# Kernel optimization log

Measured on AMD Instinct MI355X. Metric: run time of the kernel, lower is better.

The kernel has to match this reference:

```python
import jax, jax.numpy as jnp
import numpy as np

B, C, H, W = 2, 320, 48, 48
HEADS, DIM_HEAD, NUM_FILTERS = 8, 64, 32
INNER = HEADS * DIM_HEAD  # 512
LN_EPS = 1e-05


def setup_inputs() -> dict:
    key = jax.random.key(0)
    ks = jax.random.split(key, 8)
    w = 0.02
    return {
        "hidden_states": jax.random.normal(ks[0], (B, C, H, W), jnp.float32),
        "encoder_hidden_states": jax.random.normal(ks[1], (B, C, H, W), jnp.float32),
        "Wq": jax.random.normal(ks[2], (C, INNER), jnp.float32) * w,
        "Wk": jax.random.normal(ks[3], (C, INNER), jnp.float32) * w,
        "Wv": jax.random.normal(ks[4], (C, INNER), jnp.float32) * w,
        "Wo": jax.random.normal(ks[5], (INNER, C), jnp.float32) * w,
        "bo": jnp.zeros((C,), jnp.float32),
        "ln_gamma": jnp.ones((C,), jnp.float32),
        "ln_beta": jnp.zeros((C,), jnp.float32),
        "ex_filters": jax.random.normal(ks[6], (NUM_FILTERS, INNER), jnp.float32),
        "dist_filters": jax.random.normal(ks[7], (NUM_FILTERS, INNER), jnp.float32),
        "scale": jnp.ones((1,), jnp.float32),  # learnable scale shadows dim_head**-0.5
    }


def _split_heads(t, heads):
    b, s, d = t.shape
    return t.reshape(b, s, heads, d // heads).transpose(0, 2, 1, 3)  # [b,h,s,dh]


def reference(hidden_states, encoder_hidden_states, Wq, Wk, Wv, Wo, bo,
              ln_gamma, ln_beta, ex_filters, dist_filters, scale):
    b, c, h, w = hidden_states.shape
    _, _, rh, rw = encoder_hidden_states.shape
    residual = hidden_states
    s = scale[0]

    hs = hidden_states.transpose(0, 2, 3, 1).reshape(b, h * w, c)        # [b, q, C]
    ehs = encoder_hidden_states.transpose(0, 2, 3, 1).reshape(b, rh * rw, c)

    # LayerNorm on encoder states
    mu = ehs.mean(-1, keepdims=True)
    var = jnp.mean((ehs - mu) ** 2, axis=-1, keepdims=True)
    ehs = (ehs - mu) * jax.lax.rsqrt(var + LN_EPS) * ln_gamma + ln_beta

    q = _split_heads(hs @ Wq, HEADS)    # [b,h,q,dh]
    k = _split_heads(ehs @ Wk, HEADS)   # [b,h,kv,dh]
    v = _split_heads(ehs @ Wv, HEADS)   # [b,h,kv,dh]
    ef = _split_heads(jnp.broadcast_to(ex_filters[None], (b,) + ex_filters.shape), HEADS)   # [b,h,F,dh]
    df = _split_heads(jnp.broadcast_to(dist_filters[None], (b,) + dist_filters.shape), HEADS)

    # spatial attention: softmax over kv positions
    spatial = jax.nn.softmax(jnp.einsum('bhfd,bhkd->bhfk', ef, k) * s, axis=-1)   # [b,h,F,kv]
    # channel attention: softmax over the filter axis (torch dim=1 of [B*h, F, q])
    channel = jax.nn.softmax(jnp.einsum('bhfd,bhqd->bhfq', df, q) * s, axis=2)    # [b,h,F,q]

    attn = jnp.einsum('bhfq,bhfk->bhqk', channel, spatial)                        # [b,h,q,kv]
    out = jnp.einsum('bhqk,bhkd->bhqd', attn, v)                                  # [b,h,q,dh]

    out = out.transpose(0, 2, 1, 3).reshape(b, h * w, INNER)
    out = out @ Wo + bo
    out = out.reshape(b, h, w, c).transpose(0, 3, 1, 2)
    return out + residual * s
```

## Files before the change

### kernel.cpp

```cpp
#include <hip/hip_runtime.h>
#include <math.h>

#define Bc 2
#define Cc 320
#define Pc 2304
#define HEADSc 8
#define DHc 64
#define INNERc 512
#define Fc 32
#define LN_EPS 1e-5f
#define CHUNKS 36
#define CHUNK_P 64

typedef __attribute__((ext_vector_type(8))) short bf16x8;
typedef __attribute__((ext_vector_type(4))) float f32x4;

static __device__ __forceinline__ ushort f2bf(float x) {
  uint u = __builtin_bit_cast(uint, x);
  u = (u + 0x7fffu + ((u >> 16) & 1u)) >> 16;
  return (ushort)u;
}

static __device__ __forceinline__ void gload16(const ushort* g, ushort* l) {
  __builtin_amdgcn_global_load_lds(
      (const __attribute__((address_space(1))) uint*)g,
      (__attribute__((address_space(3))) uint*)l, 16, 0, 0);
}

static __device__ void transpose_tile(const float* __restrict__ src,
                                      ushort* __restrict__ dst, int R, int C,
                                      int r0, int c0, int tid,
                                      float (*t)[65]) {
#pragma unroll
  for (int it = 0; it < 4; ++it) {
    int lin = it * 256 + tid;
    int rr = lin >> 4, c4 = lin & 15;
    float4 v = *(const float4*)(&src[(size_t)(r0 + rr) * C + c0 + c4 * 4]);
    t[rr][c4 * 4 + 0] = v.x; t[rr][c4 * 4 + 1] = v.y;
    t[rr][c4 * 4 + 2] = v.z; t[rr][c4 * 4 + 3] = v.w;
  }
  __syncthreads();
#pragma unroll
  for (int it = 0; it < 2; ++it) {
    int lin = it * 256 + tid;
    int cc = lin >> 3, r8 = lin & 7;
    ushort tmp[8];
#pragma unroll
    for (int j = 0; j < 8; ++j) tmp[j] = f2bf(t[r8 * 8 + j][cc]);
    *(uint4*)(&dst[(size_t)(c0 + cc) * R + r0 + r8 * 8]) = *(const uint4*)tmp;
  }
}

__global__ __launch_bounds__(256) void prep_all_kernel(
    const float* __restrict__ hs, const float* __restrict__ ehs,
    const float* __restrict__ gamma, const float* __restrict__ beta,
    const float* __restrict__ Wv, const float* __restrict__ Wo,
    const float* __restrict__ exf, const float* __restrict__ Wk,
    const float* __restrict__ dif, const float* __restrict__ Wq,
    ushort* __restrict__ hsT, ushort* __restrict__ ehsT,
    ushort* __restrict__ WvT, ushort* __restrict__ WoT,
    ushort* __restrict__ Gk, ushort* __restrict__ Gq) {
  __shared__ float smem[6448];
  int idx = blockIdx.x, tid = threadIdx.x;

  if (idx < 144) {
    int pt = idx % 36, z = idx / 36;
    int b = z & 1, which = z >> 1;
    int pos0 = pt * 64;
    const float* src = (which ? ehs : hs) + (size_t)b * Cc * Pc;
    ushort* dst = (which ? ehsT : hsT) + (size_t)b * Pc * Cc;
    float* t = smem;
    float* s1 = smem + 4160;
    float* s2 = smem + 4416;
    float* lmean = smem + 4672;
    float* lrstd = smem + 4736;
    int lane = tid & 63, g = tid >> 6;
    if (which) {
      const float* base = src + pos0 + lane;
      float sum = 0.f, sq = 0.f;
      for (int c = g * 80; c < g * 80 + 80; ++c) {
        float x = base[(size_t)c * Pc];
        sum += x; sq += x * x;
      }
      s1[g * 64 + lane] = sum; s2[g * 64 + lane] = sq;
      __syncthreads();
      if (tid < 64) {
        float ts = s1[tid] + s1[64 + tid] + s1[128 + tid] + s1[192 + tid];
        float tq = s2[tid] + s2[64 + tid] + s2[128 + tid] + s2[192 + tid];
        float mean = ts / (float)Cc;
        float var = tq / (float)Cc - mean * mean;
        lmean[tid] = mean;
        lrstd[tid] = rsqrtf(var + LN_EPS);
      }
      __syncthreads();
    }
    float4 pv[4];
#pragma unroll
    for (int it = 0; it < 4; ++it) {
      int lin = it * 256 + tid, rr = lin >> 4, c4 = lin & 15;
      pv[it] = *(const float4*)(&src[(size_t)rr * Pc + pos0 + c4 * 4]);
    }
    for (int ct = 0; ct < 5; ++ct) {
      int r0 = ct * 64;
#pragma unroll
      for (int it = 0; it < 4; ++it) {
        int lin = it * 256 + tid, rr = lin >> 4, c4 = lin & 15;
        t[rr * 65 + c4 * 4 + 0] = pv[it].x;
        t[rr * 65 + c4 * 4 + 1] = pv[it].y;
        t[rr * 65 + c4 * 4 + 2] = pv[it].z;
        t[rr * 65 + c4 * 4 + 3] = pv[it].w;
      }
      __syncthreads();
      if (ct < 4) {
#pragma unroll
        for (int it = 0; it < 4; ++it) {
          int lin = it * 256 + tid, rr = lin >> 4, c4 = lin & 15;
          pv[it] =
              *(const float4*)(&src[(size_t)(r0 + 64 + rr) * Pc + pos0 + c4 * 4]);
        }
      }
#pragma unroll
      for (int it = 0; it < 2; ++it) {
        int lin = it * 256 + tid;
        int cc = lin >> 3, r8 = lin & 7;
        float m_ = which ? lmean[cc] : 0.f, rs_ = which ? lrstd[cc] : 1.f;
        ushort tmp[8];
#pragma unroll
        for (int j = 0; j < 8; ++j) {
          int ch = r8 * 8 + j;
          float x = t[ch * 65 + cc];
          float val = which ? (x - m_) * rs_ * gamma[r0 + ch] + beta[r0 + ch] : x;
          tmp[j] = f2bf(val);
        }
        *(uint4*)(&dst[(size_t)(pos0 + cc) * Cc + r0 + r8 * 8]) =
            *(const uint4*)tmp;
      }
      __syncthreads();
    }
  } else {
    int idx2 = idx - 144;
    if (idx2 < 40) {
      transpose_tile(Wv, WvT, Cc, INNERc, (idx2 / 8) * 64, (idx2 % 8) * 64,
                     tid, (float(*)[65])smem);
    } else if (idx2 < 80) {
      int i = idx2 - 40;
      transpose_tile(Wo, WoT, INNERc, Cc, (i / 5) * 64, (i % 5) * 64, tid,
                     (float(*)[65])smem);
    } else {
      int i = idx2 - 80;
      int c0 = (i % 5) * 64, h = (i / 5) % 8, zz = i / 40;
      const float* filt = zz ? dif : exf;
      const float* W = zz ? Wq : Wk;
      ushort* G = zz ? Gq : Gk;
      float (*ef)[66] = (float(*)[66])smem;
      float (*wk)[65] = (float(*)[65])(smem + 32 * 66);
      for (int l = tid; l < Fc * DHc; l += 256) {
        int f = l >> 6, d = l & 63;
        ef[f][d] = filt[(size_t)f * INNERc + h * 64 + d];
      }
      for (int l = tid; l < 64 * DHc; l += 256) {
        int cc = l >> 6, d = l & 63;
        wk[cc][d] = W[(size_t)(c0 + cc) * INNERc + h * 64 + d];
      }
      __syncthreads();
      int f = tid >> 3, cbase = tid & 7;
      float acc[8] = {};
#pragma unroll
      for (int d4 = 0; d4 < DHc; d4 += 4) {
        float4 a = *(const float4*)(&ef[f][d4]);
#pragma unroll
        for (int j = 0; j < 8; ++j) {
          float4 b = *(const float4*)(&wk[cbase + j * 8][d4]);
          acc[j] += a.x * b.x + a.y * b.y + a.z * b.z + a.w * b.w;
        }
      }
#pragma unroll
      for (int j = 0; j < 8; ++j)
        G[(size_t)(h * Fc + f) * Cc + c0 + cbase + j * 8] = f2bf(acc[j]);
    }
  }
}

__global__ __launch_bounds__(256) void spatial_kernel(
    const ushort* __restrict__ Gk, const ushort* __restrict__ ehsT,
    const ushort* __restrict__ WvT, const float* __restrict__ scale_p,
    float* __restrict__ svp, float* __restrict__ mj, float* __restrict__ lj) {
  int c = blockIdx.x, h = blockIdx.y, b = blockIdx.z;
  int tid = threadIdx.x, lane = tid & 63, wv = tid >> 6;
  int l15 = lane & 15, kq = lane >> 4;
  int pos0 = c * CHUNK_P;
  int bh = b * HEADSc + h;
  float s = scale_p[0];

  __shared__ alignas(16) char smem[40960];
  float* Sq = (float*)smem;
  ushort* Vs = (ushort*)(smem + 8704);
  ushort* P = (ushort*)(smem + 17920);

  const ushort* Av = WvT + (size_t)(h * 64) * Cc;
  const ushort* Ag = Gk + (size_t)(h * Fc) * Cc;
  const ushort* Bb = ehsT + ((size_t)b * Pc + pos0) * Cc;

  auto stage = [&](int buf, int k0) {
    ushort* As_ = (ushort*)(smem + buf * 20480);
    ushort* Bs_ = (ushort*)(smem + buf * 20480 + 12288);
#pragma unroll
    for (int it = 0; it < 3; ++it) {
      int lin = it * 256 + tid;
      int row = lin >> 3, p = lin & 7;
      int lc = p ^ (row & 7);
      const ushort* sp = (row < 64)
                             ? (Av + (size_t)row * Cc + k0 + lc * 8)
                             : (Ag + (size_t)(row - 64) * Cc + k0 + lc * 8);
      gload16(sp, &As_[lin * 8]);
    }
#pragma unroll
    for (int it = 0; it < 2; ++it) {
      int lin = it * 256 + tid;
      int row = lin >> 3, p = lin & 7;
      int lc = p ^ (row & 7);
      gload16(Bb + (size_t)row * Cc + k0 + lc * 8, &Bs_[lin * 8]);
    }
  };

  f32x4 acc[6] = {};
  stage(0, 0);
  __syncthreads();
  int cur = 0;
  for (int t = 0; t < 5; ++t) {
    if (t < 4) stage(cur ^ 1, (t + 1) * 64);
    const ushort* As_ = (const ushort*)(smem + cur * 20480);
    const ushort* Bs_ = (const ushort*)(smem + cur * 20480 + 12288);
#pragma unroll
    for (int ss = 0; ss < 2; ++ss) {
      bf16x8 af[6], bfr;
#pragma unroll
      for (int mt = 0; mt < 6; ++mt) {
        int m = mt * 16 + l15;
        int p = (ss * 4 + kq) ^ (m & 7);
        af[mt] = *(const bf16x8*)(&As_[m * 64 + p * 8]);
      }
      {
        int n = wv * 16 + l15;
        int p = (ss * 4 + kq) ^ (n & 7);
        bfr = *(const bf16x8*)(&Bs_[n * 64 + p * 8]);
      }
#pragma unroll
      for (int mt = 0; mt < 6; ++mt)
        acc[mt] = __builtin_amdgcn_mfma_f32_16x16x32_bf16(af[mt], bfr, acc[mt],
                                                          0, 0, 0);
    }
    __syncthreads();
    cur ^= 1;
  }
#pragma unroll
  for (int mt = 0; mt < 6; ++mt) {
    int col = wv * 16 + l15;
#pragma unroll
    for (int r = 0; r < 4; ++r) {
      int row = mt * 16 + kq * 4 + r;
      if (mt < 4) Vs[row * 72 + col] = f2bf(acc[mt][r]);
      else Sq[(row - 64) * 68 + col] = acc[mt][r];
    }
  }
  __syncthreads();

  {
    int row = tid >> 3, sub = tid & 7;
    float vals[8];
    float m_ = -1e30f;
#pragma unroll
    for (int i = 0; i < 8; ++i) {
      vals[i] = s * Sq[row * 68 + sub * 8 + i];
      m_ = fmaxf(m_, vals[i]);
    }
    m_ = fmaxf(m_, __shfl_xor(m_, 1));
    m_ = fmaxf(m_, __shfl_xor(m_, 2));
    m_ = fmaxf(m_, __shfl_xor(m_, 4));
    float l_ = 0.f;
#pragma unroll
    for (int i = 0; i < 8; i += 2) {
      float e0 = __expf(vals[i] - m_);
      float e1 = __expf(vals[i + 1] - m_);
      l_ += e0 + e1;
      uint pk = (uint)f2bf(e0) | ((uint)f2bf(e1) << 16);
      *(uint*)(&P[row * 72 + sub * 8 + i]) = pk;
    }
    l_ += __shfl_xor(l_, 1);
    l_ += __shfl_xor(l_, 2);
    l_ += __shfl_xor(l_, 4);
    if (sub == 0) {
      mj[((size_t)c * 16 + bh) * Fc + row] = m_;
      lj[((size_t)c * 16 + bh) * Fc + row] = l_;
    }
  }
  __syncthreads();

  f32x4 acc2[2] = {};
#pragma unroll
  for (int ss = 0; ss < 2; ++ss) {
    bf16x8 af[2];
#pragma unroll
    for (int mt = 0; mt < 2; ++mt)
      af[mt] = *(const bf16x8*)(&P[(mt * 16 + l15) * 72 + ss * 32 + kq * 8]);
    bf16x8 bfr = *(const bf16x8*)(&Vs[(wv * 16 + l15) * 72 + ss * 32 + kq * 8]);
#pragma unroll
    for (int mt = 0; mt < 2; ++mt)
      acc2[mt] = __builtin_amdgcn_mfma_f32_16x16x32_bf16(af[mt], bfr, acc2[mt],
                                                         0, 0, 0);
  }
  float* op = svp + ((size_t)c * 16 + bh) * (Fc * DHc);
#pragma unroll
  for (int mt = 0; mt < 2; ++mt)
#pragma unroll
    for (int r = 0; r < 4; ++r)
      op[(mt * 16 + kq * 4 + r) * DHc + wv * 16 + l15] = acc2[mt][r];
}

__global__ __launch_bounds__(256) void sv_reduce_kernel(
    const float* __restrict__ svp, const float* __restrict__ mj,
    const float* __restrict__ lj, ushort* __restrict__ svT) {
  int idx = blockIdx.x * 256 + threadIdx.x;
  int d = idx & 63, fr = idx >> 6;
  int bh = fr >> 5, f = fr & 31;
  float m = -1e30f;
#pragma unroll
  for (int c = 0; c < CHUNKS; ++c)
    m = fmaxf(m, mj[((size_t)c * 16 + bh) * Fc + f]);
  float osum = 0.f, lsum = 0.f;
#pragma unroll 4
  for (int c = 0; c < CHUNKS; ++c) {
    float w = __expf(mj[((size_t)c * 16 + bh) * Fc + f] - m);
    osum += w * svp[((size_t)c * 16 + bh) * (Fc * DHc) + f * DHc + d];
    lsum += w * lj[((size_t)c * 16 + bh) * Fc + f];
  }
  svT[((size_t)bh * DHc + d) * Fc + f] = f2bf(osum / lsum);
}

__global__ __launch_bounds__(256) void channel_kernel(
    const ushort* __restrict__ Gq, const ushort* __restrict__ hsT,
    const ushort* __restrict__ svT, const float* __restrict__ scale_p,
    ushort* __restrict__ OAT) {
  int pb = blockIdx.x, h = blockIdx.y, b = blockIdx.z;
  int pos0 = pb * 64;
  int tid = threadIdx.x, lane = tid & 63, wv = tid >> 6;
  int l15 = lane & 15, kq = lane >> 4;
  float s = scale_p[0];

  __shared__ alignas(16) char smem[28672];
  float* SO = (float*)smem;
  ushort* Pt = (ushort*)(smem + 17408);
  ushort* svs = (ushort*)(smem + 22528);
  float* red = (float*)(smem + 27648);

  const ushort* Bb = hsT + ((size_t)b * Pc + pos0) * Cc;
  const ushort* Ab = Gq + (size_t)(h * Fc) * Cc;

  auto stage = [&](int buf, int k0) {
    ushort* Aq_ = (ushort*)(smem + buf * 12288);
    ushort* Bs_ = (ushort*)(smem + buf * 12288 + 4096);
    {
      int lin = tid, row = lin >> 3, p = lin & 7;
      int lc = p ^ (row & 7);
      gload16(Ab + (size_t)row * Cc + k0 + lc * 8, &Aq_[lin * 8]);
    }
#pragma unroll
    for (int it = 0; it < 2; ++it) {
      int lin = it * 256 + tid, row = lin >> 3, p = lin & 7;
      int lc = p ^ (row & 7);
      gload16(Bb + (size_t)row * Cc + k0 + lc * 8, &Bs_[lin * 8]);
    }
  };

  f32x4 acc[2] = {};
  stage(0, 0);
  __syncthreads();
  int cur = 0;
  for (int t = 0; t < 5; ++t) {
    if (t < 4) stage(cur ^ 1, (t + 1) * 64);
    const ushort* Aq_ = (const ushort*)(smem + cur * 12288);
    const ushort* Bs_ = (const ushort*)(smem + cur * 12288 + 4096);
#pragma unroll
    for (int ss = 0; ss < 2; ++ss) {
      int n = wv * 16 + l15;
      int pb_ = (ss * 4 + kq) ^ (n & 7);
      bf16x8 bfr = *(const bf16x8*)(&Bs_[n * 64 + pb_ * 8]);
#pragma unroll
      for (int mt = 0; mt < 2; ++mt) {
        int m = mt * 16 + l15;
        int pa = (ss * 4 + kq) ^ (m & 7);
        bf16x8 af = *(const bf16x8*)(&Aq_[m * 64 + pa * 8]);
        acc[mt] = __builtin_amdgcn_mfma_f32_16x16x32_bf16(af, bfr, acc[mt],
                                                          0, 0, 0);
      }
    }
    __syncthreads();
    cur ^= 1;
  }

#pragma unroll
  for (int mt = 0; mt < 2; ++mt)
#pragma unroll
    for (int r = 0; r < 4; ++r)
      SO[(mt * 16 + kq * 4 + r) * 68 + wv * 16 + l15] = acc[mt][r];
  {
    int rr = tid >> 2, p = tid & 3;
    *(uint4*)(&svs[rr * 40 + p * 8]) = *(const uint4*)(
        svT + ((size_t)(b * HEADSc + h) * DHc + rr) * Fc + p * 8);
  }
  __syncthreads();
  {
    int pos = tid & 63, g = tid >> 6;
    float v8[8];
    float pm = -1e30f;
#pragma unroll
    for (int i = 0; i < 8; ++i) {
      v8[i] = s * SO[(g * 8 + i) * 68 + pos];
      pm = fmaxf(pm, v8[i]);
    }
    red[g * 64 + pos] = pm;
    __syncthreads();
    float m_ = fmaxf(fmaxf(red[pos], red[64 + pos]),
                     fmaxf(red[128 + pos], red[192 + pos]));
    __syncthreads();
    float ps = 0.f;
#pragma unroll
    for (int i = 0; i < 8; ++i) {
      v8[i] = __expf(v8[i] - m_);
      ps += v8[i];
    }
    red[g * 64 + pos] = ps;
    __syncthreads();
    float inv = 1.f / (red[pos] + red[64 + pos] + red[128 + pos] +
                       red[192 + pos]);
#pragma unroll
    for (int i = 0; i < 8; i += 2) {
      uint pk = (uint)f2bf(v8[i] * inv) | ((uint)f2bf(v8[i + 1] * inv) << 16);
      *(uint*)(&Pt[pos * 40 + g * 8 + i]) = pk;
    }
  }
  __syncthreads();
  {
    bf16x8 b_ = *(const bf16x8*)(&svs[(wv * 16 + l15) * 40 + kq * 8]);
    f32x4 acc3[4];
#pragma unroll
    for (int mt = 0; mt < 4; ++mt) {
      bf16x8 a_ = *(const bf16x8*)(&Pt[(mt * 16 + l15) * 40 + kq * 8]);
      f32x4 z = {0.f, 0.f, 0.f, 0.f};
      acc3[mt] = __builtin_amdgcn_mfma_f32_16x16x32_bf16(a_, b_, z, 0, 0, 0);
    }
#pragma unroll
    for (int mt = 0; mt < 4; ++mt)
#pragma unroll
      for (int r = 0; r < 4; ++r)
        SO[(mt * 16 + kq * 4 + r) * 68 + wv * 16 + l15] = acc3[mt][r];
  }
  __syncthreads();
#pragma unroll
  for (int it = 0; it < 2; ++it) {
    int lin = it * 256 + tid;
    int p = lin >> 3, c8 = lin & 7;
    ushort tmp[8];
#pragma unroll
    for (int j = 0; j < 8; ++j) tmp[j] = f2bf(SO[p * 68 + c8 * 8 + j]);
    *(uint4*)(&OAT[((size_t)b * Pc + pos0 + p) * INNERc + h * 64 + c8 * 8]) =
        *(const uint4*)tmp;
  }
}

__global__ __launch_bounds__(256) void gemm_mfma_kernel(
    const ushort* __restrict__ A, const ushort* __restrict__ Bt,
    float* __restrict__ Out, int K, int Mdim,
    const float* __restrict__ bias, const float* __restrict__ res,
    const float* __restrict__ scale_p) {
  int b = blockIdx.z;
  int n0 = blockIdx.x * 64, m0 = blockIdx.y * 64;
  int tid = threadIdx.x, lane = tid & 63, wv = tid >> 6;
  int l15 = lane & 15, kq = lane >> 4;
  __shared__ alignas(16) char smem[32768];
  const ushort* Ab = A + (size_t)m0 * K;
  const ushort* Bb = Bt + ((size_t)b * Pc + n0) * K;

  auto stage = [&](int buf, int k0) {
    ushort* As_ = (ushort*)(smem + buf * 16384);
    ushort* Bs_ = (ushort*)(smem + buf * 16384 + 8192);
#pragma unroll
    for (int it = 0; it < 2; ++it) {
      int lin = it * 256 + tid, row = lin >> 3, p = lin & 7;
      int lc = p ^ (row & 7);
      gload16(Ab + (size_t)row * K + k0 + lc * 8, &As_[lin * 8]);
    }
#pragma unroll
    for (int it = 0; it < 2; ++it) {
      int lin = it * 256 + tid, row = lin >> 3, p = lin & 7;
      int lc = p ^ (row & 7);
      gload16(Bb + (size_t)row * K + k0 + lc * 8, &Bs_[lin * 8]);
    }
  };

  f32x4 acc[4] = {};
  stage(0, 0);
  __syncthreads();
  int cur = 0;
  const int NT = K >> 6;
  for (int t = 0; t < NT; ++t) {
    if (t < NT - 1) stage(cur ^ 1, (t + 1) * 64);
    const ushort* As_ = (const ushort*)(smem + cur * 16384);
    const ushort* Bs_ = (const ushort*)(smem + cur * 16384 + 8192);
#pragma unroll
    for (int ss = 0; ss < 2; ++ss) {
      bf16x8 af[4], bfr;
#pragma unroll
      for (int mt = 0; mt < 4; ++mt) {
        int m = mt * 16 + l15;
        int p = (ss * 4 + kq) ^ (m & 7);
        af[mt] = *(const bf16x8*)(&As_[m * 64 + p * 8]);
      }
      {
        int n = wv * 16 + l15;
        int p = (ss * 4 + kq) ^ (n & 7);
        bfr = *(const bf16x8*)(&Bs_[n * 64 + p * 8]);
      }
#pragma unroll
      for (int mt = 0; mt < 4; ++mt)
        acc[mt] = __builtin_amdgcn_mfma_f32_16x16x32_bf16(af[mt], bfr, acc[mt],
                                                          0, 0, 0);
    }
    __syncthreads();
    cur ^= 1;
  }
  float s = scale_p[0];
  float* Ob = Out + ((size_t)b * Mdim + m0) * Pc + n0;
  const float* rb = res + ((size_t)b * Mdim + m0) * Pc + n0;
  int ncol = wv * 16 + l15;
#pragma unroll
  for (int mt = 0; mt < 4; ++mt)
#pragma unroll
    for (int r = 0; r < 4; ++r) {
      int m = mt * 16 + kq * 4 + r;
      Ob[(size_t)m * Pc + ncol] =
          acc[mt][r] + bias[m0 + m] + s * rb[(size_t)m * Pc + ncol];
    }
}

extern "C" void kernel_launch(void* const* d_in, const int* in_sizes, int n_in,
                              void* d_out, int out_size, void* d_ws, size_t ws_size,
                              hipStream_t stream) {
  const float* hs    = (const float*)d_in[0];
  const float* ehs   = (const float*)d_in[1];
  const float* Wq    = (const float*)d_in[2];
  const float* Wk    = (const float*)d_in[3];
  const float* Wv    = (const float*)d_in[4];
  const float* Wo    = (const float*)d_in[5];
  const float* bo    = (const float*)d_in[6];
  const float* gamma = (const float*)d_in[7];
  const float* beta  = (const float*)d_in[8];
  const float* exf   = (const float*)d_in[9];
  const float* dif   = (const float*)d_in[10];
  const float* scale = (const float*)d_in[11];
  float* out = (float*)d_out;

  float* ws = (float*)d_ws;
  float* svp = ws;
  float* mj  = svp + 1179648;
  float* lj  = mj + 18432;
  ushort* hsT  = (ushort*)(lj + 18432);
  ushort* ehsT = hsT + 1474560;
  ushort* WvT  = ehsT + 1474560;
  ushort* WoT  = WvT + 163840;
  ushort* Gk   = WoT + 163840;
  ushort* Gq   = Gk + 81920;
  ushort* svT  = Gq + 81920;
  ushort* OAT  = svT + 32768;

  prep_all_kernel<<<dim3(304), dim3(256), 0, stream>>>(
      hs, ehs, gamma, beta, Wv, Wo, exf, Wk, dif, Wq,
      hsT, ehsT, WvT, WoT, Gk, Gq);
  spatial_kernel<<<dim3(CHUNKS, HEADSc, Bc), dim3(256), 0, stream>>>(
      Gk, ehsT, WvT, scale, svp, mj, lj);
  sv_reduce_kernel<<<dim3(128), dim3(256), 0, stream>>>(svp, mj, lj, svT);
  channel_kernel<<<dim3(Pc / 64, HEADSc, Bc), dim3(256), 0, stream>>>(
      Gq, hsT, svT, scale, OAT);
  gemm_mfma_kernel<<<dim3(Pc / 64, Cc / 64, Bc), dim3(256), 0, stream>>>(
      WoT, OAT, out, INNERc, Cc, bo, hs, scale);
}
```

Measured before the change: 132.1 us.

## Merge spatial and channel passes into one launch, fuse P·sv into output GEMM

```diff
diff --git a/kernel.cpp b/kernel.cpp
--- a/kernel.cpp
+++ b/kernel.cpp
@@ -181,140 +181,241 @@
   }
 }
 
-__global__ __launch_bounds__(256) void spatial_kernel(
+__global__ __launch_bounds__(256) void mid_kernel(
     const ushort* __restrict__ Gk, const ushort* __restrict__ ehsT,
-    const ushort* __restrict__ WvT, const float* __restrict__ scale_p,
-    float* __restrict__ svp, float* __restrict__ mj, float* __restrict__ lj) {
-  int c = blockIdx.x, h = blockIdx.y, b = blockIdx.z;
+    const ushort* __restrict__ WvT, const ushort* __restrict__ Gq,
+    const ushort* __restrict__ hsT, const float* __restrict__ scale_p,
+    float* __restrict__ svp, float* __restrict__ mj, float* __restrict__ lj,
+    ushort* __restrict__ Pn) {
+  __shared__ alignas(16) char smem[40960];
   int tid = threadIdx.x, lane = tid & 63, wv = tid >> 6;
   int l15 = lane & 15, kq = lane >> 4;
-  int pos0 = c * CHUNK_P;
-  int bh = b * HEADSc + h;
+  int typ = (int)blockIdx.x & 1, sidx = (int)blockIdx.x >> 1;
   float s = scale_p[0];
 
-  __shared__ alignas(16) char smem[40960];
-  float* Sq = (float*)smem;
-  ushort* Vs = (ushort*)(smem + 8704);
-  ushort* P = (ushort*)(smem + 17920);
-
-  const ushort* Av = WvT + (size_t)(h * 64) * Cc;
-  const ushort* Ag = Gk + (size_t)(h * Fc) * Cc;
-  const ushort* Bb = ehsT + ((size_t)b * Pc + pos0) * Cc;
-
-  auto stage = [&](int buf, int k0) {
-    ushort* As_ = (ushort*)(smem + buf * 20480);
-    ushort* Bs_ = (ushort*)(smem + buf * 20480 + 12288);
-#pragma unroll
-    for (int it = 0; it < 3; ++it) {
-      int lin = it * 256 + tid;
-      int row = lin >> 3, p = lin & 7;
-      int lc = p ^ (row & 7);
-      const ushort* sp = (row < 64)
-                             ? (Av + (size_t)row * Cc + k0 + lc * 8)
-                             : (Ag + (size_t)(row - 64) * Cc + k0 + lc * 8);
-      gload16(sp, &As_[lin * 8]);
-    }
-#pragma unroll
-    for (int it = 0; it < 2; ++it) {
-      int lin = it * 256 + tid;
-      int row = lin >> 3, p = lin & 7;
-      int lc = p ^ (row & 7);
-      gload16(Bb + (size_t)row * Cc + k0 + lc * 8, &Bs_[lin * 8]);
-    }
-  };
-
-  f32x4 acc[6] = {};
-  stage(0, 0);
-  __syncthreads();
-  int cur = 0;
-  for (int t = 0; t < 5; ++t) {
-    if (t < 4) stage(cur ^ 1, (t + 1) * 64);
-    const ushort* As_ = (const ushort*)(smem + cur * 20480);
-    const ushort* Bs_ = (const ushort*)(smem + cur * 20480 + 12288);
+  if (typ == 0) {
+    int c = sidx % 36, h = (sidx / 36) & 7, b = sidx / 288;
+    int pos0 = c * CHUNK_P;
+    int bh = b * HEADSc + h;
+    float* Sq = (float*)smem;
+    ushort* Vs = (ushort*)(smem + 8704);
+    ushort* P = (ushort*)(smem + 17920);
+
+    const ushort* Av = WvT + (size_t)(h * 64) * Cc;
+    const ushort* Ag = Gk + (size_t)(h * Fc) * Cc;
+    const ushort* Bb = ehsT + ((size_t)b * Pc + pos0) * Cc;
+
+    auto stage = [&](int buf, int k0) {
+      ushort* As_ = (ushort*)(smem + buf * 20480);
+      ushort* Bs_ = (ushort*)(smem + buf * 20480 + 12288);
+#pragma unroll
+      for (int it = 0; it < 3; ++it) {
+        int lin = it * 256 + tid;
+        int row = lin >> 3, p = lin & 7;
+        int lc = p ^ (row & 7);
+        const ushort* sp = (row < 64)
+                               ? (Av + (size_t)row * Cc + k0 + lc * 8)
+                               : (Ag + (size_t)(row - 64) * Cc + k0 + lc * 8);
+        gload16(sp, &As_[lin * 8]);
+      }
+#pragma unroll
+      for (int it = 0; it < 2; ++it) {
+        int lin = it * 256 + tid;
+        int row = lin >> 3, p = lin & 7;
+        int lc = p ^ (row & 7);
+        gload16(Bb + (size_t)row * Cc + k0 + lc * 8, &Bs_[lin * 8]);
+      }
+    };
+
+    f32x4 acc[6] = {};
+    stage(0, 0);
+    __syncthreads();
+    int cur = 0;
+    for (int t = 0; t < 5; ++t) {
+      if (t < 4) stage(cur ^ 1, (t + 1) * 64);
+      const ushort* As_ = (const ushort*)(smem + cur * 20480);
+      const ushort* Bs_ = (const ushort*)(smem + cur * 20480 + 12288);
+#pragma unroll
+      for (int ss = 0; ss < 2; ++ss) {
+        bf16x8 af[6], bfr;
+#pragma unroll
+        for (int mt = 0; mt < 6; ++mt) {
+          int m = mt * 16 + l15;
+          int p = (ss * 4 + kq) ^ (m & 7);
+          af[mt] = *(const bf16x8*)(&As_[m * 64 + p * 8]);
+        }
+        {
+          int n = wv * 16 + l15;
+          int p = (ss * 4 + kq) ^ (n & 7);
+          bfr = *(const bf16x8*)(&Bs_[n * 64 + p * 8]);
+        }
+#pragma unroll
+        for (int mt = 0; mt < 6; ++mt)
+          acc[mt] = __builtin_amdgcn_mfma_f32_16x16x32_bf16(af[mt], bfr,
+                                                            acc[mt], 0, 0, 0);
+      }
+      __syncthreads();
+      cur ^= 1;
+    }
+#pragma unroll
+    for (int mt = 0; mt < 6; ++mt) {
+      int col = wv * 16 + l15;
+#pragma unroll
+      for (int r = 0; r < 4; ++r) {
+        int row = mt * 16 + kq * 4 + r;
+        if (mt < 4) Vs[row * 72 + col] = f2bf(acc[mt][r]);
+        else Sq[(row - 64) * 68 + col] = acc[mt][r];
+      }
+    }
+    __syncthreads();
+
+    {
+      int row = tid >> 3, sub = tid & 7;
+      float vals[8];
+      float m_ = -1e30f;
+#pragma unroll
+      for (int i = 0; i < 8; ++i) {
+        vals[i] = s * Sq[row * 68 + sub * 8 + i];
+        m_ = fmaxf(m_, vals[i]);
+      }
+      m_ = fmaxf(m_, __shfl_xor(m_, 1));
+      m_ = fmaxf(m_, __shfl_xor(m_, 2));
+      m_ = fmaxf(m_, __shfl_xor(m_, 4));
+      float l_ = 0.f;
+#pragma unroll
+      for (int i = 0; i < 8; i += 2) {
+        float e0 = __expf(vals[i] - m_);
+        float e1 = __expf(vals[i + 1] - m_);
+        l_ += e0 + e1;
+        uint pk = (uint)f2bf(e0) | ((uint)f2bf(e1) << 16);
+        *(uint*)(&P[row * 72 + sub * 8 + i]) = pk;
+      }
+      l_ += __shfl_xor(l_, 1);
+      l_ += __shfl_xor(l_, 2);
+      l_ += __shfl_xor(l_, 4);
+      if (sub == 0) {
+        mj[((size_t)c * 16 + bh) * Fc + row] = m_;
+        lj[((size_t)c * 16 + bh) * Fc + row] = l_;
+      }
+    }
+    __syncthreads();
+
+    f32x4 acc2[2] = {};
 #pragma unroll
     for (int ss = 0; ss < 2; ++ss) {
-      bf16x8 af[6], bfr;
-#pragma unroll
-      for (int mt = 0; mt < 6; ++mt) {
-        int m = mt * 16 + l15;
-        int p = (ss * 4 + kq) ^ (m & 7);
-        af[mt] = *(const bf16x8*)(&As_[m * 64 + p * 8]);
-      }
+      bf16x8 af[2];
+#pragma unroll
+      for (int mt = 0; mt < 2; ++mt)
+        af[mt] = *(const bf16x8*)(&P[(mt * 16 + l15) * 72 + ss * 32 + kq * 8]);
+      bf16x8 bfr =
+          *(const bf16x8*)(&Vs[(wv * 16 + l15) * 72 + ss * 32 + kq * 8]);
+#pragma unroll
+      for (int mt = 0; mt < 2; ++mt)
+        acc2[mt] = __builtin_amdgcn_mfma_f32_16x16x32_bf16(af[mt], bfr,
+                                                           acc2[mt], 0, 0, 0);
+    }
+    float* op = svp + ((size_t)c * 16 + bh) * (Fc * DHc);
+#pragma unroll
+    for (int mt = 0; mt < 2; ++mt)
+#pragma unroll
+      for (int r = 0; r < 4; ++r)
+        op[(mt * 16 + kq * 4 + r) * DHc + wv * 16 + l15] = acc2[mt][r];
+  } else {
+    int pb = sidx % 36, h = (sidx / 36) & 7, b = sidx / 288;
+    int pos0 = pb * 64;
+    float* SO = (float*)smem;
+    ushort* Pt = (ushort*)(smem + 17408);
+    float* red = (float*)(smem + 22528);
+
+    const ushort* Bb = hsT + ((size_t)b * Pc + pos0) * Cc;
+    const ushort* Ab = Gq + (size_t)(h * Fc) * Cc;
+
+    auto stage = [&](int buf, int k0) {
+      ushort* Aq_ = (ushort*)(smem + buf * 12288);
+      ushort* Bs_ = (ushort*)(smem + buf * 12288 + 4096);
       {
+        int lin = tid, row = lin >> 3, p = lin & 7;
+        int lc = p ^ (row & 7);
+        gload16(Ab + (size_t)row * Cc + k0 + lc * 8, &Aq_[lin * 8]);
+      }
+#pragma unroll
+      for (int it = 0; it < 2; ++it) {
+        int lin = it * 256 + tid, row = lin >> 3, p = lin & 7;
+        int lc = p ^ (row & 7);
+        gload16(Bb + (size_t)row * Cc + k0 + lc * 8, &Bs_[lin * 8]);
+      }
+    };
+
+    f32x4 acc[2] = {};
+    stage(0, 0);
+    __syncthreads();
+    int cur = 0;
+    for (int t = 0; t < 5; ++t) {
+      if (t < 4) stage(cur ^ 1, (t + 1) * 64);
+      const ushort* Aq_ = (const ushort*)(smem + cur * 12288);
+      const ushort* Bs_ = (const ushort*)(smem + cur * 12288 + 4096);
+#pragma unroll
+      for (int ss = 0; ss < 2; ++ss) {
         int n = wv * 16 + l15;
-        int p = (ss * 4 + kq) ^ (n & 7);
-        bfr = *(const bf16x8*)(&Bs_[n * 64 + p * 8]);
-      }
-#pragma unroll
-      for (int mt = 0; mt < 6; ++mt)
-        acc[mt] = __builtin_amdgcn_mfma_f32_16x16x32_bf16(af[mt], bfr, acc[mt],
-                                                          0, 0, 0);
-    }
-    __syncthreads();
-    cur ^= 1;
+        int pb_ = (ss * 4 + kq) ^ (n & 7);
+        bf16x8 bfr = *(const bf16x8*)(&Bs_[n * 64 + pb_ * 8]);
+#pragma unroll
+        for (int mt = 0; mt < 2; ++mt) {
+          int m = mt * 16 + l15;
+          int pa = (ss * 4 + kq) ^ (m & 7);
+          bf16x8 af = *(const bf16x8*)(&Aq_[m * 64 + pa * 8]);
+          acc[mt] = __builtin_amdgcn_mfma_f32_16x16x32_bf16(af, bfr, acc[mt],
+                                                            0, 0, 0);
+        }
+      }
+      __syncthreads();
+      cur ^= 1;
+    }
+
+#pragma unroll
+    for (int mt = 0; mt < 2; ++mt)
+#pragma unroll
+      for (int r = 0; r < 4; ++r)
+        SO[(mt * 16 + kq * 4 + r) * 68 + wv * 16 + l15] = acc[mt][r];
+    __syncthreads();
+    {
+      int pos = tid & 63, g = tid >> 6;
+      float v8[8];
+      float pm = -1e30f;
+#pragma unroll
+      for (int i = 0; i < 8; ++i) {
+        v8[i] = s * SO[(g * 8 + i) * 68 + pos];
+        pm = fmaxf(pm, v8[i]);
+      }
+      red[g * 64 + pos] = pm;
+      __syncthreads();
+      float m_ = fmaxf(fmaxf(red[pos], red[64 + pos]),
+                       fmaxf(red[128 + pos], red[192 + pos]));
+      __syncthreads();
+      float ps = 0.f;
+#pragma unroll
+      for (int i = 0; i < 8; ++i) {
+        v8[i] = __expf(v8[i] - m_);
+        ps += v8[i];
+      }
+      red[g * 64 + pos] = ps;
+      __syncthreads();
+      float inv = 1.f / (red[pos] + red[64 + pos] + red[128 + pos] +
+                         red[192 + pos]);
+#pragma unroll
+      for (int i = 0; i < 8; i += 2) {
+        uint pk =
+            (uint)f2bf(v8[i] * inv) | ((uint)f2bf(v8[i + 1] * inv) << 16);
+        *(uint*)(&Pt[pos * 40 + g * 8 + i]) = pk;
+      }
+    }
+    __syncthreads();
+    {
+      int p = tid >> 2, ch = tid & 3;
+      *(uint4*)(&Pn[((size_t)(b * HEADSc + h) * Pc + pos0 + p) * Fc +
+                    ch * 8]) = *(const uint4*)(&Pt[p * 40 + ch * 8]);
+    }
   }
-#pragma unroll
-  for (int mt = 0; mt < 6; ++mt) {
-    int col = wv * 16 + l15;
-#pragma unroll
-    for (int r = 0; r < 4; ++r) {
-      int row = mt * 16 + kq * 4 + r;
-      if (mt < 4) Vs[row * 72 + col] = f2bf(acc[mt][r]);
-      else Sq[(row - 64) * 68 + col] = acc[mt][r];
-    }
-  }
-  __syncthreads();
-
-  {
-    int row = tid >> 3, sub = tid & 7;
-    float vals[8];
-    float m_ = -1e30f;
-#pragma unroll
-    for (int i = 0; i < 8; ++i) {
-      vals[i] = s * Sq[row * 68 + sub * 8 + i];
-      m_ = fmaxf(m_, vals[i]);
-    }
-    m_ = fmaxf(m_, __shfl_xor(m_, 1));
-    m_ = fmaxf(m_, __shfl_xor(m_, 2));
-    m_ = fmaxf(m_, __shfl_xor(m_, 4));
-    float l_ = 0.f;
-#pragma unroll
-    for (int i = 0; i < 8; i += 2) {
-      float e0 = __expf(vals[i] - m_);
-      float e1 = __expf(vals[i + 1] - m_);
-      l_ += e0 + e1;
-      uint pk = (uint)f2bf(e0) | ((uint)f2bf(e1) << 16);
-      *(uint*)(&P[row * 72 + sub * 8 + i]) = pk;
-    }
-    l_ += __shfl_xor(l_, 1);
-    l_ += __shfl_xor(l_, 2);
-    l_ += __shfl_xor(l_, 4);
-    if (sub == 0) {
-      mj[((size_t)c * 16 + bh) * Fc + row] = m_;
-      lj[((size_t)c * 16 + bh) * Fc + row] = l_;
-    }
-  }
-  __syncthreads();
-
-  f32x4 acc2[2] = {};
-#pragma unroll
-  for (int ss = 0; ss < 2; ++ss) {
-    bf16x8 af[2];
-#pragma unroll
-    for (int mt = 0; mt < 2; ++mt)
-      af[mt] = *(const bf16x8*)(&P[(mt * 16 + l15) * 72 + ss * 32 + kq * 8]);
-    bf16x8 bfr = *(const bf16x8*)(&Vs[(wv * 16 + l15) * 72 + ss * 32 + kq * 8]);
-#pragma unroll
-    for (int mt = 0; mt < 2; ++mt)
-      acc2[mt] = __builtin_amdgcn_mfma_f32_16x16x32_bf16(af[mt], bfr, acc2[mt],
-                                                         0, 0, 0);
-  }
-  float* op = svp + ((size_t)c * 16 + bh) * (Fc * DHc);
-#pragma unroll
-  for (int mt = 0; mt < 2; ++mt)
-#pragma unroll
-    for (int r = 0; r < 4; ++r)
-      op[(mt * 16 + kq * 4 + r) * DHc + wv * 16 + l15] = acc2[mt][r];
 }
 
 __global__ __launch_bounds__(256) void sv_reduce_kernel(
@@ -337,176 +438,56 @@
   svT[((size_t)bh * DHc + d) * Fc + f] = f2bf(osum / lsum);
 }
 
-__global__ __launch_bounds__(256) void channel_kernel(
-    const ushort* __restrict__ Gq, const ushort* __restrict__ hsT,
+__global__ __launch_bounds__(256) void pvgemm_kernel(
+    const ushort* __restrict__ WoT, const ushort* __restrict__ Pn,
     const ushort* __restrict__ svT, const float* __restrict__ scale_p,
-    ushort* __restrict__ OAT) {
-  int pb = blockIdx.x, h = blockIdx.y, b = blockIdx.z;
-  int pos0 = pb * 64;
+    const float* __restrict__ bias, const float* __restrict__ res,
+    float* __restrict__ Out) {
+  int n0 = blockIdx.x * 64, m0 = blockIdx.y * 64, b = blockIdx.z;
   int tid = threadIdx.x, lane = tid & 63, wv = tid >> 6;
   int l15 = lane & 15, kq = lane >> 4;
-  float s = scale_p[0];
-
-  __shared__ alignas(16) char smem[28672];
-  float* SO = (float*)smem;
-  ushort* Pt = (ushort*)(smem + 17408);
-  ushort* svs = (ushort*)(smem + 22528);
-  float* red = (float*)(smem + 27648);
-
-  const ushort* Bb = hsT + ((size_t)b * Pc + pos0) * Cc;
-  const ushort* Ab = Gq + (size_t)(h * Fc) * Cc;
-
-  auto stage = [&](int buf, int k0) {
-    ushort* Aq_ = (ushort*)(smem + buf * 12288);
-    ushort* Bs_ = (ushort*)(smem + buf * 12288 + 4096);
-    {
-      int lin = tid, row = lin >> 3, p = lin & 7;
-      int lc = p ^ (row & 7);
-      gload16(Ab + (size_t)row * Cc + k0 + lc * 8, &Aq_[lin * 8]);
-    }
+  __shared__ alignas(16) char smem[24576];
+  ushort* As = (ushort*)smem;
+  ushort* Pns = (ushort*)(smem + 8192);
+  ushort* svs = (ushort*)(smem + 12288);
+  ushort* Vb = (ushort*)(smem + 16384);
+
+  f32x4 acc[4] = {};
+  for (int h = 0; h < HEADSc; ++h) {
+    const ushort* Ab = WoT + (size_t)m0 * INNERc + h * 64;
+    const ushort* Pb = Pn + ((size_t)(b * HEADSc + h) * Pc + n0) * Fc;
+    const ushort* Sb = svT + (size_t)(b * HEADSc + h) * DHc * Fc;
 #pragma unroll
     for (int it = 0; it < 2; ++it) {
       int lin = it * 256 + tid, row = lin >> 3, p = lin & 7;
-      int lc = p ^ (row & 7);
-      gload16(Bb + (size_t)row * Cc + k0 + lc * 8, &Bs_[lin * 8]);
-    }
-  };
-
-  f32x4 acc[2] = {};
-  stage(0, 0);
-  __syncthreads();
-  int cur = 0;
-  for (int t = 0; t < 5; ++t) {
-    if (t < 4) stage(cur ^ 1, (t + 1) * 64);
-    const ushort* Aq_ = (const ushort*)(smem + cur * 12288);
-    const ushort* Bs_ = (const ushort*)(smem + cur * 12288 + 4096);
-#pragma unroll
-    for (int ss = 0; ss < 2; ++ss) {
-      int n = wv * 16 + l15;
-      int pb_ = (ss * 4 + kq) ^ (n & 7);
-      bf16x8 bfr = *(const bf16x8*)(&Bs_[n * 64 + pb_ * 8]);
-#pragma unroll
-      for (int mt = 0; mt < 2; ++mt) {
-        int m = mt * 16 + l15;
-        int pa = (ss * 4 + kq) ^ (m & 7);
-        bf16x8 af = *(const bf16x8*)(&Aq_[m * 64 + pa * 8]);
-        acc[mt] = __builtin_amdgcn_mfma_f32_16x16x32_bf16(af, bfr, acc[mt],
-                                                          0, 0, 0);
-      }
-    }
-    __syncthreads();
-    cur ^= 1;
-  }
-
-#pragma unroll
-  for (int mt = 0; mt < 2; ++mt)
-#pragma unroll
-    for (int r = 0; r < 4; ++r)
-      SO[(mt * 16 + kq * 4 + r) * 68 + wv * 16 + l15] = acc[mt][r];
-  {
-    int rr = tid >> 2, p = tid & 3;
-    *(uint4*)(&svs[rr * 40 + p * 8]) = *(const uint4*)(
-        svT + ((size_t)(b * HEADSc + h) * DHc + rr) * Fc + p * 8);
-  }
-  __syncthreads();
-  {
-    int pos = tid & 63, g = tid >> 6;
-    float v8[8];
-    float pm = -1e30f;
-#pragma unroll
-    for (int i = 0; i < 8; ++i) {
-      v8[i] = s * SO[(g * 8 + i) * 68 + pos];
-      pm = fmaxf(pm, v8[i]);
-    }
-    red[g * 64 + pos] = pm;
-    __syncthreads();
-    float m_ = fmaxf(fmaxf(red[pos], red[64 + pos]),
-                     fmaxf(red[128 + pos], red[192 + pos]));
-    __syncthreads();
-    float ps = 0.f;
-#pragma unroll
-    for (int i = 0; i < 8; ++i) {
-      v8[i] = __expf(v8[i] - m_);
-      ps += v8[i];
-    }
-    red[g * 64 + pos] = ps;
-    __syncthreads();
-    float inv = 1.f / (red[pos] + red[64 + pos] + red[128 + pos] +
-                       red[192 + pos]);
-#pragma unroll
-    for (int i = 0; i < 8; i += 2) {
-      uint pk = (uint)f2bf(v8[i] * inv) | ((uint)f2bf(v8[i + 1] * inv) << 16);
-      *(uint*)(&Pt[pos * 40 + g * 8 + i]) = pk;
-    }
-  }
-  __syncthreads();
-  {
-    bf16x8 b_ = *(const bf16x8*)(&svs[(wv * 16 + l15) * 40 + kq * 8]);
-    f32x4 acc3[4];
-#pragma unroll
-    for (int mt = 0; mt < 4; ++mt) {
-      bf16x8 a_ = *(const bf16x8*)(&Pt[(mt * 16 + l15) * 40 + kq * 8]);
-      f32x4 z = {0.f, 0.f, 0.f, 0.f};
-      acc3[mt] = __builtin_amdgcn_mfma_f32_16x16x32_bf16(a_, b_, z, 0, 0, 0);
-    }
-#pragma unroll
-    for (int mt = 0; mt < 4; ++mt)
-#pragma unroll
-      for (int r = 0; r < 4; ++r)
-        SO[(mt * 16 + kq * 4 + r) * 68 + wv * 16 + l15] = acc3[mt][r];
-  }
-  __syncthreads();
-#pragma unroll
-  for (int it = 0; it < 2; ++it) {
-    int lin = it * 256 + tid;
-    int p = lin >> 3, c8 = lin & 7;
-    ushort tmp[8];
-#pragma unroll
-    for (int j = 0; j < 8; ++j) tmp[j] = f2bf(SO[p * 68 + c8 * 8 + j]);
-    *(uint4*)(&OAT[((size_t)b * Pc + pos0 + p) * INNERc + h * 64 + c8 * 8]) =
-        *(const uint4*)tmp;
-  }
-}
-
-__global__ __launch_bounds__(256) void gemm_mfma_kernel(
-    const ushort* __restrict__ A, const ushort* __restrict__ Bt,
-    float* __restrict__ Out, int K, int Mdim,
-    const float* __restrict__ bias, const float* __restrict__ res,
-    const float* __restrict__ scale_p) {
-  int b = blockIdx.z;
-  int n0 = blockIdx.x * 64, m0 = blockIdx.y * 64;
-  int tid = threadIdx.x, lane = tid & 63, wv = tid >> 6;
-  int l15 = lane & 15, kq = lane >> 4;
-  __shared__ alignas(16) char smem[32768];
-  const ushort* Ab = A + (size_t)m0 * K;
-  const ushort* Bb = Bt + ((size_t)b * Pc + n0) * K;
-
-  auto stage = [&](int buf, int k0) {
-    ushort* As_ = (ushort*)(smem + buf * 16384);
-    ushort* Bs_ = (ushort*)(smem + buf * 16384 + 8192);
-#pragma unroll
-    for (int it = 0; it < 2; ++it) {
-      int lin = it * 256 + tid, row = lin >> 3, p = lin & 7;
-      int lc = p ^ (row & 7);
-      gload16(Ab + (size_t)row * K + k0 + lc * 8, &As_[lin * 8]);
-    }
-#pragma unroll
-    for (int it = 0; it < 2; ++it) {
-      int lin = it * 256 + tid, row = lin >> 3, p = lin & 7;
-      int lc = p ^ (row & 7);
-      gload16(Bb + (size_t)row * K + k0 + lc * 8, &Bs_[lin * 8]);
-    }
-  };
-
-  f32x4 acc[4] = {};
-  stage(0, 0);
-  __syncthreads();
-  int cur = 0;
-  const int NT = K >> 6;
-  for (int t = 0; t < NT; ++t) {
-    if (t < NT - 1) stage(cur ^ 1, (t + 1) * 64);
-    const ushort* As_ = (const ushort*)(smem + cur * 16384);
-    const ushort* Bs_ = (const ushort*)(smem + cur * 16384 + 8192);
+      gload16(Ab + (size_t)row * INNERc + ((p ^ (row & 7)) * 8), &As[lin * 8]);
+    }
+    {
+      int row = tid >> 2, p = tid & 3;
+      gload16(Pb + (size_t)row * Fc + ((p ^ (row & 3)) * 8), &Pns[tid * 8]);
+    }
+    {
+      int row = tid >> 2, p = tid & 3;
+      gload16(Sb + (size_t)row * Fc + ((p ^ (row & 3)) * 8), &svs[tid * 8]);
+    }
+    __syncthreads();
+    {
+      int m = wv * 16 + l15;
+      bf16x8 af = *(const bf16x8*)(&Pns[m * 32 + ((kq ^ (m & 3)) * 8)]);
+#pragma unroll
+      for (int nt = 0; nt < 4; ++nt) {
+        int n = nt * 16 + l15;
+        bf16x8 bfv = *(const bf16x8*)(&svs[n * 32 + ((kq ^ (n & 3)) * 8)]);
+        f32x4 z = {0.f, 0.f, 0.f, 0.f};
+        f32x4 d4 = __builtin_amdgcn_mfma_f32_16x16x32_bf16(af, bfv, z, 0, 0, 0);
+#pragma unroll
+        for (int r = 0; r < 4; ++r) {
+          int pos = wv * 16 + kq * 4 + r, d = nt * 16 + l15;
+          Vb[pos * 64 + (((d >> 3) ^ (pos & 7)) * 8) + (d & 7)] = f2bf(d4[r]);
+        }
+      }
+    }
+    __syncthreads();
 #pragma unroll
     for (int ss = 0; ss < 2; ++ss) {
       bf16x8 af[4], bfr;
@@ -514,12 +495,12 @@
       for (int mt = 0; mt < 4; ++mt) {
         int m = mt * 16 + l15;
         int p = (ss * 4 + kq) ^ (m & 7);
-        af[mt] = *(const bf16x8*)(&As_[m * 64 + p * 8]);
+        af[mt] = *(const bf16x8*)(&As[m * 64 + p * 8]);
       }
       {
         int n = wv * 16 + l15;
         int p = (ss * 4 + kq) ^ (n & 7);
-        bfr = *(const bf16x8*)(&Bs_[n * 64 + p * 8]);
+        bfr = *(const bf16x8*)(&Vb[n * 64 + p * 8]);
       }
 #pragma unroll
       for (int mt = 0; mt < 4; ++mt)
@@ -527,11 +508,10 @@
                                                           0, 0, 0);
     }
     __syncthreads();
-    cur ^= 1;
   }
   float s = scale_p[0];
-  float* Ob = Out + ((size_t)b * Mdim + m0) * Pc + n0;
-  const float* rb = res + ((size_t)b * Mdim + m0) * Pc + n0;
+  float* Ob = Out + ((size_t)b * Cc + m0) * Pc + n0;
+  const float* rb = res + ((size_t)b * Cc + m0) * Pc + n0;
   int ncol = wv * 16 + l15;
 #pragma unroll
   for (int mt = 0; mt < 4; ++mt)
@@ -571,16 +551,14 @@
   ushort* Gk   = WoT + 163840;
   ushort* Gq   = Gk + 81920;
   ushort* svT  = Gq + 81920;
-  ushort* OAT  = svT + 32768;
+  ushort* Pn   = svT + 32768;
 
   prep_all_kernel<<<dim3(304), dim3(256), 0, stream>>>(
       hs, ehs, gamma, beta, Wv, Wo, exf, Wk, dif, Wq,
       hsT, ehsT, WvT, WoT, Gk, Gq);
-  spatial_kernel<<<dim3(CHUNKS, HEADSc, Bc), dim3(256), 0, stream>>>(
-      Gk, ehsT, WvT, scale, svp, mj, lj);
+  mid_kernel<<<dim3(1152), dim3(256), 0, stream>>>(
+      Gk, ehsT, WvT, Gq, hsT, scale, svp, mj, lj, Pn);
   sv_reduce_kernel<<<dim3(128), dim3(256), 0, stream>>>(svp, mj, lj, svT);
-  channel_kernel<<<dim3(Pc / 64, HEADSc, Bc), dim3(256), 0, stream>>>(
-      Gq, hsT, svT, scale, OAT);
-  gemm_mfma_kernel<<<dim3(Pc / 64, Cc / 64, Bc), dim3(256), 0, stream>>>(
-      WoT, OAT, out, INNERc, Cc, bo, hs, scale);
-}
+  pvgemm_kernel<<<dim3(Pc / 64, Cc / 64, Bc), dim3(256), 0, stream>>>(
+      WoT, Pn, svT, scale, bo, hs, out);
+}
```

Result: slower. 137.9 us (+4.4%).
